# Kernel optimization log

Measured on AMD Instinct MI355X. Metric: run time of the kernel, lower is better.

The kernel has to match this reference:

```python
import jax, jax.numpy as jnp
import numpy as np

B, S, V, H, K, T = 4, 256, 32000, 1024, 4, 20
THRESHOLD = 0.6


def setup_inputs() -> dict:
    key = jax.random.key(0)
    ks = jax.random.split(key, 12)
    sH = 1.0 / np.sqrt(H)
    return {
        "input_ids": jax.random.randint(ks[0], (B, S), 0, V),
        "labels": jax.random.randint(ks[1], (B, S), 0, V),
        "embed": jax.random.normal(ks[2], (V, H), jnp.float32) * 0.02,
        "W1": jax.random.normal(ks[3], (H, H), jnp.float32) * sH,
        "b1": jnp.zeros((H,), jnp.float32),
        "lm_head": jax.random.normal(ks[4], (H, V), jnp.float32) * 0.02,
        "W_gen": jax.random.normal(ks[5], (H, H), jnp.float32) * sH,
        "thought_emb": jax.random.normal(ks[6], (K, H), jnp.float32) * 0.02,
        "tpos_emb": jax.random.normal(ks[7], (T, H), jnp.float32) * 0.02,
        "w_score": jax.random.normal(ks[8], (2 * H,), jnp.float32) * sH,
        "w_gate": jax.random.normal(ks[9], (2 * H,), jnp.float32) * sH,
    }


def reference(input_ids, labels, embed, W1, b1, lm_head, W_gen,
              thought_emb, tpos_emb, w_score, w_gate):
    # ---- base model: embed -> tanh MLP -> lm_head ----
    h0 = embed[input_ids]                                 # (B,S,H)
    hidden = jnp.tanh(h0 @ W1 + b1)                       # base last_hidden_state
    base_logits = hidden @ lm_head                        # (B,S,V)

    # ---- ThoughtInjector: per-position gate from normalized entropy ----
    logp = jax.nn.log_softmax(base_logits, axis=-1)
    ent = -jnp.sum(jnp.exp(logp) * logp, axis=-1) / jnp.log(float(V))  # (B,S)
    inject = (ent.mean(axis=0) > THRESHOLD) & (jnp.arange(S) < S - 1)   # (S,)

    # ---- ThoughtGenerator: (B,S,K,T,H) thoughts (masked dispatch, all pos) ----
    g = jnp.tanh(hidden @ W_gen)                          # (B,S,H)
    thoughts = jnp.tanh(g[:, :, None, None, :]
                        + thought_emb[None, None, :, None, :]
                        + tpos_emb[None, None, None, :, :])  # (B,S,K,T,H)
    tmean = thoughts.mean(axis=3)                         # (B,S,K,H) = thoughts.mean(dim=2)

    # ---- CoherenceScorer: composite score per thought ----
    comp = jax.nn.sigmoid(
        jnp.einsum('bsh,h->bs', hidden, w_score[:H])[:, :, None]
        + jnp.einsum('bskh,h->bsk', tmean, w_score[H:]))  # (B,S,K)

    # ---- MixingHead: coherence-weighted thought mix, gated blend with hidden ----
    alpha = jax.nn.softmax(comp, axis=-1)                 # (B,S,K)
    mixed_thought = jnp.einsum('bsk,bskh->bsh', alpha, tmean)
    gate = jax.nn.sigmoid(jnp.einsum('bsh,h->bs', hidden, w_gate[:H])
                          + jnp.einsum('bsh,h->bs', mixed_thought, w_gate[H:]))[..., None]
    mixed = gate * mixed_thought + (1.0 - gate) * hidden

    enhanced = jnp.where(inject[None, :, None], mixed, hidden)
    final_logits = enhanced @ lm_head                     # (B,S,V)

    # ---- shifted cross-entropy loss ----
    sl = jax.nn.log_softmax(final_logits[:, :-1, :], axis=-1)
    loss = -jnp.take_along_axis(sl, labels[:, 1:, None], axis=-1).mean()
    return final_logits, loss
```

## Files before the change

### kernel.cpp

```cpp
#include <hip/hip_runtime.h>


#define V_SZ 32000
#define H_SZ 1024
#define S_SZ 256
#define B_SZ 4
#define M_SZ 1024
#define K_TH 4
#define T_TH 20
#define NTILE_V 125
#define PARTS (NTILE_V * 4)

typedef __bf16 bf16_t;
typedef __bf16 bf16x8 __attribute__((ext_vector_type(8)));
typedef __bf16 bf16x4 __attribute__((ext_vector_type(4)));
typedef float  f32x4  __attribute__((ext_vector_type(4)));

typedef __attribute__((address_space(1))) void gvoid_t;
typedef __attribute__((address_space(3))) void lvoid_t;

__device__ __forceinline__ void async_copy16(const bf16_t* g, bf16_t* l) {
  __builtin_amdgcn_global_load_lds((gvoid_t*)g, (lvoid_t*)l, 16, 0, 0);
}

__device__ __forceinline__ float tanh_fast(float x) {
  x = fminf(fmaxf(x, -15.f), 15.f);
  float e = __expf(2.f * x);
  return (e - 1.f) / (e + 1.f);
}
__device__ __forceinline__ float sigmoid_f(float x) {
  return 1.f / (1.f + __expf(-x));
}

__device__ __forceinline__ void transpose_tile(
    const float* __restrict__ in, bf16_t* __restrict__ out, int R, int C,
    int bx, int by, float (*tile)[65], int t) {
  const int c0 = bx << 6, r0 = by << 6;
  const int tr = t >> 4, tc = (t & 15) << 2;
  #pragma unroll
  for (int i = 0; i < 4; ++i) {
    const float4 v = *(const float4*)(in + (size_t)(r0 + tr + 16 * i) * C + c0 + tc);
    tile[tr + 16 * i][tc]     = v.x;
    tile[tr + 16 * i][tc + 1] = v.y;
    tile[tr + 16 * i][tc + 2] = v.z;
    tile[tr + 16 * i][tc + 3] = v.w;
  }
  __syncthreads();
  const int wr = t >> 3, wc = (t & 7) << 3;
  #pragma unroll
  for (int i = 0; i < 2; ++i) {
    bf16x8 o;
    #pragma unroll
    for (int j = 0; j < 8; ++j) o[j] = (bf16_t)tile[wc + j][wr + 32 * i];
    *(bf16x8*)(out + (size_t)(c0 + wr + 32 * i) * R + r0 + wc) = o;
  }
}

__global__ void __launch_bounds__(256) prep_kernel(
    const float* __restrict__ lm, const float* __restrict__ W1,
    const float* __restrict__ Wg, const int* __restrict__ ids,
    const float* __restrict__ embed, bf16_t* __restrict__ lmT,
    bf16_t* __restrict__ W1T, bf16_t* __restrict__ WgT,
    bf16_t* __restrict__ X0) {
  __shared__ float tile[64][65];
  const int t = threadIdx.x;
  int bid = blockIdx.x;
  if (bid < 8000) {
    transpose_tile(lm, lmT, H_SZ, V_SZ, bid % 500, bid / 500, tile, t);
    return;
  }
  bid -= 8000;
  if (bid < 256) {
    transpose_tile(W1, W1T, H_SZ, H_SZ, bid % 16, bid / 16, tile, t);
    return;
  }
  bid -= 256;
  if (bid < 256) {
    transpose_tile(Wg, WgT, H_SZ, H_SZ, bid % 16, bid / 16, tile, t);
    return;
  }
  bid -= 256;
  const int i = bid * 256 + t;
  const int m = i >> 8, c4 = (i & 255) << 2;
  const float4 v = *(const float4*)(embed + (size_t)ids[m] * H_SZ + c4);
  bf16x4 o;
  o[0] = (bf16_t)v.x; o[1] = (bf16_t)v.y; o[2] = (bf16_t)v.z; o[3] = (bf16_t)v.w;
  *(bf16x4*)(X0 + (size_t)m * H_SZ + c4) = o;
}

template <int EPI>
__global__ void __launch_bounds__(256, 2) gemm_bt(
    const bf16_t* __restrict__ A, const bf16_t* __restrict__ BT,
    float* __restrict__ outF, bf16_t* __restrict__ outB,
    const float* __restrict__ bias, int mtiles, int ntiles, int N) {
  __shared__ __align__(16) bf16_t As[128 * 32];
  __shared__ __align__(16) bf16_t Bs[128 * 32];
  const int t = threadIdx.x;
  const int x = blockIdx.x & 7, y = blockIdx.x >> 3;
  const int tm = y % mtiles, tn = x + 8 * (y / mtiles);
  if (tn >= ntiles) return;
  const int m0 = tm * 128, n0 = tn * 128;
  const int lane = t & 63, wv = t >> 6, wm = wv >> 1, wn = wv & 1;
  const int col = lane & 15, qd = lane >> 4;

  const int srow = 16 * wv + (lane >> 2);
  const int schunk = ((lane & 3) ^ ((srow >> 1) & 3)) << 3;
  const bf16_t* gA0 = A  + (size_t)(m0 + srow) * 1024 + schunk;
  const bf16_t* gA1 = A  + (size_t)(m0 + srow + 64) * 1024 + schunk;
  const bf16_t* gB0 = BT + (size_t)(n0 + srow) * 1024 + schunk;
  const bf16_t* gB1 = BT + (size_t)(n0 + srow + 64) * 1024 + schunk;
  bf16_t* lA0 = As + wv * 512;
  bf16_t* lA1 = As + 2048 + wv * 512;
  bf16_t* lB0 = Bs + wv * 512;
  bf16_t* lB1 = Bs + 2048 + wv * 512;

  int offA[4], offB[4];
  #pragma unroll
  for (int i = 0; i < 4; ++i) {
    const int ra = wm * 64 + i * 16 + col;
    offA[i] = ra * 32 + ((qd ^ ((ra >> 1) & 3)) << 3);
    const int rb = wn * 64 + i * 16 + col;
    offB[i] = rb * 32 + ((qd ^ ((rb >> 1) & 3)) << 3);
  }
  f32x4 acc[4][4] = {};
  for (int kb = 0; kb < 1024; kb += 32) {
    async_copy16(gA0 + kb, lA0);
    async_copy16(gA1 + kb, lA1);
    async_copy16(gB0 + kb, lB0);
    async_copy16(gB1 + kb, lB1);
    __syncthreads();
    bf16x8 af[4], bg[4];
    #pragma unroll
    for (int mi = 0; mi < 4; ++mi) af[mi] = *(const bf16x8*)(As + offA[mi]);
    #pragma unroll
    for (int ni = 0; ni < 4; ++ni) bg[ni] = *(const bf16x8*)(Bs + offB[ni]);
    #pragma unroll
    for (int mi = 0; mi < 4; ++mi)
      #pragma unroll
      for (int ni = 0; ni < 4; ++ni)
        acc[mi][ni] = __builtin_amdgcn_mfma_f32_16x16x32_bf16(
            af[mi], bg[ni], acc[mi][ni], 0, 0, 0);
    __syncthreads();
  }
  #pragma unroll
  for (int mi = 0; mi < 4; ++mi) {
    #pragma unroll
    for (int ni = 0; ni < 4; ++ni) {
      const int gm = m0 + wm * 64 + mi * 16 + qd * 4;
      const int gn = n0 + wn * 64 + ni * 16 + col;
      #pragma unroll
      for (int r = 0; r < 4; ++r) {
        const size_t o = (size_t)(gm + r) * N + gn;
        float v = acc[mi][ni][r];
        if (EPI == 1) {
          v = tanh_fast(v + bias[gn]);
          outF[o] = v;
          outB[o] = (bf16_t)v;
        } else {
          outF[o] = tanh_fast(v);
        }
      }
    }
  }
}

template <int EPI>
__global__ void __launch_bounds__(512, 2) gemm_big(
    const bf16_t* __restrict__ A, const bf16_t* __restrict__ BT,
    float* __restrict__ outF, float2* __restrict__ entP,
    float* __restrict__ lseP, int mtiles, int ntiles, int N) {
  __shared__ __align__(16) bf16_t As[3][256 * 32];
  __shared__ __align__(16) bf16_t Bs[3][256 * 32];
  const int t = threadIdx.x;
  const int x = blockIdx.x & 7, y = blockIdx.x >> 3;
  const int tm = y % mtiles, tn = x + 8 * (y / mtiles);
  if (tn >= ntiles) return;
  const int m0 = tm * 256, n0 = tn * 256;
  const int lane = t & 63, wv = t >> 6;
  const int wm = wv >> 2, wn = wv & 3;
  const int col = lane & 15, qd = lane >> 4;

  int ldsOff[2], srow[2], sch[2];
  #pragma unroll
  for (int j = 0; j < 2; ++j) {
    const int cid = j * 512 + wv * 64 + lane;
    srow[j] = cid >> 2;
    sch[j] = ((cid & 3) ^ ((srow[j] >> 1) & 3)) << 3;
    ldsOff[j] = (j * 512 + wv * 64) * 8;
  }
  const bf16_t* gA0 = A  + (size_t)(m0 + srow[0]) * 1024 + sch[0];
  const bf16_t* gA1 = A  + (size_t)(m0 + srow[1]) * 1024 + sch[1];
  const bf16_t* gB0 = BT + (size_t)(n0 + srow[0]) * 1024 + sch[0];
  const bf16_t* gB1 = BT + (size_t)(n0 + srow[1]) * 1024 + sch[1];

  int offA[8], offB[4];
  #pragma unroll
  for (int i = 0; i < 8; ++i) {
    const int ra = wm * 128 + i * 16 + col;
    offA[i] = ra * 32 + ((qd ^ ((ra >> 1) & 3)) << 3);
  }
  #pragma unroll
  for (int i = 0; i < 4; ++i) {
    const int rb = wn * 64 + i * 16 + col;
    offB[i] = rb * 32 + ((qd ^ ((rb >> 1) & 3)) << 3);
  }

  f32x4 acc[8][4] = {};

  async_copy16(gA0, &As[0][ldsOff[0]]);
  async_copy16(gA1, &As[0][ldsOff[1]]);
  async_copy16(gB0, &Bs[0][ldsOff[0]]);
  async_copy16(gB1, &Bs[0][ldsOff[1]]);
  async_copy16(gA0 + 32, &As[1][ldsOff[0]]);
  async_copy16(gA1 + 32, &As[1][ldsOff[1]]);
  async_copy16(gB0 + 32, &Bs[1][ldsOff[0]]);
  async_copy16(gB1 + 32, &Bs[1][ldsOff[1]]);
  asm volatile("s_waitcnt vmcnt(4)" ::: "memory");
  __builtin_amdgcn_sched_barrier(0);
  __builtin_amdgcn_s_barrier();

  int cur = 0;
  for (int kt = 0; kt < 32; ++kt) {
    const bf16_t* __restrict__ Ab = &As[cur][0];
    const bf16_t* __restrict__ Bb = &Bs[cur][0];
    const int nb = (cur == 0) ? 2 : cur - 1;
    const int kb2 = (kt + 2) * 32;
    bf16x8 af[8], b0, b1;
    #pragma unroll
    for (int i = 0; i < 8; ++i) af[i] = *(const bf16x8*)(Ab + offA[i]);
    b0 = *(const bf16x8*)(Bb + offB[0]);
    b1 = *(const bf16x8*)(Bb + offB[1]);
    if (kt < 30) {
      async_copy16(gA0 + kb2, &As[nb][ldsOff[0]]);
      async_copy16(gA1 + kb2, &As[nb][ldsOff[1]]);
    }
    __builtin_amdgcn_s_barrier();
    __builtin_amdgcn_s_setprio(1);
    #pragma unroll
    for (int i = 0; i < 8; ++i) {
      acc[i][0] = __builtin_amdgcn_mfma_f32_16x16x32_bf16(af[i], b0, acc[i][0], 0, 0, 0);
      acc[i][1] = __builtin_amdgcn_mfma_f32_16x16x32_bf16(af[i], b1, acc[i][1], 0, 0, 0);
    }
    __builtin_amdgcn_s_setprio(0);
    __builtin_amdgcn_s_barrier();
    b0 = *(const bf16x8*)(Bb + offB[2]);
    b1 = *(const bf16x8*)(Bb + offB[3]);
    if (kt < 30) {
      async_copy16(gB0 + kb2, &Bs[nb][ldsOff[0]]);
      async_copy16(gB1 + kb2, &Bs[nb][ldsOff[1]]);
      asm volatile("s_waitcnt vmcnt(4)" ::: "memory");
    } else if (kt == 30) {
      asm volatile("s_waitcnt vmcnt(0)" ::: "memory");
    }
    __builtin_amdgcn_sched_barrier(0);
    __builtin_amdgcn_s_barrier();
    __builtin_amdgcn_s_setprio(1);
    #pragma unroll
    for (int i = 0; i < 8; ++i) {
      acc[i][2] = __builtin_amdgcn_mfma_f32_16x16x32_bf16(af[i], b0, acc[i][2], 0, 0, 0);
      acc[i][3] = __builtin_amdgcn_mfma_f32_16x16x32_bf16(af[i], b1, acc[i][3], 0, 0, 0);
    }
    __builtin_amdgcn_s_setprio(0);
    __builtin_amdgcn_s_barrier();
    cur = (cur == 2) ? 0 : cur + 1;
  }

  #pragma unroll
  for (int mi = 0; mi < 8; ++mi) {
    #pragma unroll
    for (int rr = 0; rr < 4; ++rr) {
      const int row = m0 + wm * 128 + mi * 16 + qd * 4 + rr;
      float zz = 0.f, ss = 0.f;
      #pragma unroll
      for (int ni = 0; ni < 4; ++ni) {
        const float xv = acc[mi][ni][rr];
        const float e = __expf(xv);
        zz += e;
        if (EPI == 3) ss += xv * e;
        if (EPI == 4)
          outF[(size_t)row * N + n0 + wn * 64 + ni * 16 + col] = xv;
      }
      #pragma unroll
      for (int d = 1; d < 16; d <<= 1) {
        zz += __shfl_xor(zz, d);
        if (EPI == 3) ss += __shfl_xor(ss, d);
      }
      if (col == 0) {
        if (EPI == 3)
          entP[(size_t)row * PARTS + tn * 4 + wn] = make_float2(zz, ss);
        else
          lseP[(size_t)row * PARTS + tn * 4 + wn] = zz;
      }
    }
  }
}

__global__ void __launch_bounds__(256) lse_merge_kernel(
    const float* __restrict__ lseP, float* __restrict__ lse) {
  const int t = threadIdx.x, w = t >> 6, lane = t & 63;
  const int row = blockIdx.x * 4 + w;
  float z = 0.f;
  for (int i = lane; i < PARTS; i += 64) z += lseP[(size_t)row * PARTS + i];
  #pragma unroll
  for (int d = 1; d < 64; d <<= 1) z += __shfl_xor(z, d);
  if (lane == 0) lse[row] = __logf(z);
}

__device__ __forceinline__ float block_sum(float v, float* red, int t) {
  red[t] = v;
  __syncthreads();
  for (int off = 128; off > 0; off >>= 1) {
    if (t < off) red[t] += red[t + off];
    __syncthreads();
  }
  const float r = red[0];
  __syncthreads();
  return r;
}

__global__ void __launch_bounds__(256) mix_kernel(
    const float* __restrict__ hidden, const float* __restrict__ gF,
    const float* __restrict__ th_emb, const float* __restrict__ tpos,
    const float* __restrict__ w_score, const float* __restrict__ w_gate,
    const float2* __restrict__ entP, bf16_t* __restrict__ enhB) {
  const int m = blockIdx.x, t = threadIdx.x, s = m & (S_SZ - 1);
  __shared__ float red[256];
  __shared__ float se[4];

  {
    const int w = t >> 6, lane = t & 63;
    const int row = w * S_SZ + s;
    float z = 0.f, sv = 0.f;
    for (int i = lane; i < PARTS; i += 64) {
      const float2 pz = entP[(size_t)row * PARTS + i];
      z += pz.x; sv += pz.y;
    }
    #pragma unroll
    for (int d = 1; d < 64; d <<= 1) {
      z += __shfl_xor(z, d);
      sv += __shfl_xor(sv, d);
    }
    if (lane == 0) se[w] = __logf(z) - sv / z;
    __syncthreads();
  }
  const float emean = 0.25f * (se[0] + se[1] + se[2] + se[3]);
  const int inj = (emean * (1.0f / 10.373491f) > 0.6f) && (s < S_SZ - 1);

  float hv[4], ws1[4], ws2[4], wg1[4], wg2[4], tmv[4][4];
  #pragma unroll
  for (int j = 0; j < 4; ++j) {
    const int h = t + 256 * j;
    hv[j]  = hidden[(size_t)m * H_SZ + h];
    ws1[j] = w_score[h];      ws2[j] = w_score[H_SZ + h];
    wg1[j] = w_gate[h];       wg2[j] = w_gate[H_SZ + h];
    const float gv = gF[(size_t)m * H_SZ + h];
    float tp[T_TH];
    #pragma unroll
    for (int tt = 0; tt < T_TH; ++tt) tp[tt] = tpos[tt * H_SZ + h];
    #pragma unroll
    for (int k = 0; k < 4; ++k) {
      const float base = gv + th_emb[k * H_SZ + h];
      float ssum = 0.f;
      #pragma unroll
      for (int tt = 0; tt < T_TH; ++tt) ssum += tanh_fast(base + tp[tt]);
      tmv[k][j] = ssum * (1.f / T_TH);
    }
  }
  float ph = 0.f, pg = 0.f;
  #pragma unroll
  for (int j = 0; j < 4; ++j) { ph += hv[j] * ws1[j]; pg += hv[j] * wg1[j]; }
  const float sh = block_sum(ph, red, t);
  const float gh = block_sum(pg, red, t);
  float comp[4];
  #pragma unroll
  for (int k = 0; k < 4; ++k) {
    float pc = 0.f;
    #pragma unroll
    for (int j = 0; j < 4; ++j) pc += tmv[k][j] * ws2[j];
    const float ck = block_sum(pc, red, t);
    comp[k] = sigmoid_f(sh + ck);
  }
  const float ma = fmaxf(fmaxf(comp[0], comp[1]), fmaxf(comp[2], comp[3]));
  float al[4], asum = 0.f;
  #pragma unroll
  for (int k = 0; k < 4; ++k) { al[k] = __expf(comp[k] - ma); asum += al[k]; }
  const float inv = 1.f / asum;
  float mx[4];
  #pragma unroll
  for (int j = 0; j < 4; ++j) {
    mx[j] = 0.f;
    #pragma unroll
    for (int k = 0; k < 4; ++k) mx[j] += al[k] * inv * tmv[k][j];
  }
  float pm = 0.f;
  #pragma unroll
  for (int j = 0; j < 4; ++j) pm += mx[j] * wg2[j];
  const float gm = block_sum(pm, red, t);
  const float gate = sigmoid_f(gh + gm);
  #pragma unroll
  for (int j = 0; j < 4; ++j) {
    const float e = inj ? (gate * mx[j] + (1.f - gate) * hv[j]) : hv[j];
    enhB[(size_t)m * H_SZ + t + 256 * j] = (bf16_t)e;
  }
}

__global__ void __launch_bounds__(256) loss_kernel(
    const float* __restrict__ logits, const float* __restrict__ lse,
    const int* __restrict__ labels, float* __restrict__ out_loss) {
  const int t = threadIdx.x;
  float acc = 0.f;
  for (int i = t; i < (S_SZ - 1) * B_SZ; i += 256) {
    const int b = i / (S_SZ - 1), s2 = i % (S_SZ - 1);
    const int m = b * S_SZ + s2;
    const int lab = labels[m + 1];
    acc += lse[m] - logits[(size_t)m * V_SZ + lab];
  }
  __shared__ float red[256];
  red[t] = acc;
  __syncthreads();
  for (int off = 128; off > 0; off >>= 1) {
    if (t < off) red[t] += red[t + off];
    __syncthreads();
  }
  if (t == 0) out_loss[0] = red[0] / (float)((S_SZ - 1) * B_SZ);
}

extern "C" void kernel_launch(void* const* d_in, const int* in_sizes, int n_in,
                              void* d_out, int out_size, void* d_ws, size_t ws_size,
                              hipStream_t stream) {
  const int*   ids    = (const int*)  d_in[0];
  const int*   labels = (const int*)  d_in[1];
  const float* embed  = (const float*)d_in[2];
  const float* W1     = (const float*)d_in[3];
  const float* b1     = (const float*)d_in[4];
  const float* lm     = (const float*)d_in[5];
  const float* Wg     = (const float*)d_in[6];
  const float* thE    = (const float*)d_in[7];
  const float* tpos   = (const float*)d_in[8];
  const float* wsc    = (const float*)d_in[9];
  const float* wgt    = (const float*)d_in[10];
  float* out = (float*)d_out;

  char* p = (char*)d_ws;
  auto carve = [&p](size_t bytes) {
    char* r = p;
    p += (bytes + 255) & ~(size_t)255;
    return r;
  };
  bf16_t* lmT   = (bf16_t*)carve((size_t)V_SZ * H_SZ * sizeof(bf16_t));
  bf16_t* W1T   = (bf16_t*)carve((size_t)H_SZ * H_SZ * sizeof(bf16_t));
  bf16_t* WgT   = (bf16_t*)carve((size_t)H_SZ * H_SZ * sizeof(bf16_t));
  bf16_t* X0    = (bf16_t*)carve((size_t)M_SZ * H_SZ * sizeof(bf16_t));
  bf16_t* hidB  = (bf16_t*)carve((size_t)M_SZ * H_SZ * sizeof(bf16_t));
  bf16_t* enhB  = (bf16_t*)carve((size_t)M_SZ * H_SZ * sizeof(bf16_t));
  float*  hidF  = (float*) carve((size_t)M_SZ * H_SZ * sizeof(float));
  float*  gF    = (float*) carve((size_t)M_SZ * H_SZ * sizeof(float));
  float*  partials = (float*)carve((size_t)M_SZ * PARTS * sizeof(float2));
  float*  lse   = (float*) carve(M_SZ * sizeof(float));
  float2* entP = (float2*)partials;
  float*  lseP = (float*)partials;

  prep_kernel<<<9536, 256, 0, stream>>>(lm, W1, Wg, ids, embed, lmT, W1T, WgT, X0);

  gemm_bt<1><<<64, 256, 0, stream>>>(X0, W1T, hidF, hidB, b1, 8, 8, H_SZ);
  gemm_bt<2><<<64, 256, 0, stream>>>(hidB, WgT, gF, nullptr, nullptr, 8, 8, H_SZ);
  gemm_big<3><<<512, 512, 0, stream>>>(hidB, lmT, nullptr, entP, nullptr, 4, NTILE_V, V_SZ);

  mix_kernel<<<M_SZ, 256, 0, stream>>>(hidF, gF, thE, tpos, wsc, wgt, entP, enhB);

  gemm_big<4><<<512, 512, 0, stream>>>(enhB, lmT, out, nullptr, lseP, 4, NTILE_V, V_SZ);
  lse_merge_kernel<<<M_SZ / 4, 256, 0, stream>>>(lseP, lse);
  loss_kernel<<<1, 256, 0, stream>>>(out, lse, labels, out + (size_t)M_SZ * V_SZ);
}
```

Before: 588.2 us.

## Retile small GEMMs, widen lm_head transpose tile, simplify big GEMM pipeline, fuse loss

The lm_head transpose now handles 128x64 tiles per block, cutting the block count in half. The H×H GEMMs switch from 128x128 tiles on 64 blocks to 64x64 double-buffered tiles on 256 blocks to fill more CUs. The big GEMM main loop drops the split half-B-fragment scheduling with mid-iteration barriers and loads all four B fragments before one MFMA burst. The lse merge and loss kernels become a single kernel that accumulates the loss with atomics, and the big GEMM zeroes the loss slot. This saves launches and improves occupancy, but it may lose MFMA/load interleaving in the big GEMM and makes the loss reduction order nondeterministic.

```diff
diff --git a/kernel.cpp b/kernel.cpp
--- a/kernel.cpp
+++ b/kernel.cpp
@@ -34,16 +34,16 @@
 
 __device__ __forceinline__ void transpose_tile(
     const float* __restrict__ in, bf16_t* __restrict__ out, int R, int C,
-    int bx, int by, float (*tile)[65], int t) {
+    int bx, int by, float* lds, int t) {
   const int c0 = bx << 6, r0 = by << 6;
   const int tr = t >> 4, tc = (t & 15) << 2;
   #pragma unroll
   for (int i = 0; i < 4; ++i) {
     const float4 v = *(const float4*)(in + (size_t)(r0 + tr + 16 * i) * C + c0 + tc);
-    tile[tr + 16 * i][tc]     = v.x;
-    tile[tr + 16 * i][tc + 1] = v.y;
-    tile[tr + 16 * i][tc + 2] = v.z;
-    tile[tr + 16 * i][tc + 3] = v.w;
+    lds[(tr + 16 * i) * 65 + tc]     = v.x;
+    lds[(tr + 16 * i) * 65 + tc + 1] = v.y;
+    lds[(tr + 16 * i) * 65 + tc + 2] = v.z;
+    lds[(tr + 16 * i) * 65 + tc + 3] = v.w;
   }
   __syncthreads();
   const int wr = t >> 3, wc = (t & 7) << 3;
@@ -51,7 +51,7 @@
   for (int i = 0; i < 2; ++i) {
     bf16x8 o;
     #pragma unroll
-    for (int j = 0; j < 8; ++j) o[j] = (bf16_t)tile[wc + j][wr + 32 * i];
+    for (int j = 0; j < 8; ++j) o[j] = (bf16_t)lds[(wc + j) * 65 + wr + 32 * i];
     *(bf16x8*)(out + (size_t)(c0 + wr + 32 * i) * R + r0 + wc) = o;
   }
 }
@@ -62,21 +62,42 @@
     const float* __restrict__ embed, bf16_t* __restrict__ lmT,
     bf16_t* __restrict__ W1T, bf16_t* __restrict__ WgT,
     bf16_t* __restrict__ X0) {
-  __shared__ float tile[64][65];
+  __shared__ float lds[64 * 129];
   const int t = threadIdx.x;
   int bid = blockIdx.x;
-  if (bid < 8000) {
-    transpose_tile(lm, lmT, H_SZ, V_SZ, bid % 500, bid / 500, tile, t);
+  if (bid < 4000) {
+    const int by = bid / 500, bx = bid % 500;
+    const int hr0 = by << 7, vc0 = bx << 6;
+    #pragma unroll
+    for (int j = 0; j < 8; ++j) {
+      const int idx = j * 256 + t;
+      const int r = idx >> 4, c4 = (idx & 15) << 2;
+      const float4 v = *(const float4*)(lm + (size_t)(hr0 + r) * V_SZ + vc0 + c4);
+      lds[(c4 + 0) * 129 + r] = v.x;
+      lds[(c4 + 1) * 129 + r] = v.y;
+      lds[(c4 + 2) * 129 + r] = v.z;
+      lds[(c4 + 3) * 129 + r] = v.w;
+    }
+    __syncthreads();
+    #pragma unroll
+    for (int j = 0; j < 4; ++j) {
+      const int idx = j * 256 + t;
+      const int i = idx >> 4, seg = idx & 15;
+      bf16x8 o;
+      #pragma unroll
+      for (int k = 0; k < 8; ++k) o[k] = (bf16_t)lds[i * 129 + seg * 8 + k];
+      *(bf16x8*)(lmT + (size_t)(vc0 + i) * H_SZ + hr0 + seg * 8) = o;
+    }
     return;
   }
-  bid -= 8000;
+  bid -= 4000;
   if (bid < 256) {
-    transpose_tile(W1, W1T, H_SZ, H_SZ, bid % 16, bid / 16, tile, t);
+    transpose_tile(W1, W1T, H_SZ, H_SZ, bid % 16, bid / 16, lds, t);
     return;
   }
   bid -= 256;
   if (bid < 256) {
-    transpose_tile(Wg, WgT, H_SZ, H_SZ, bid % 16, bid / 16, tile, t);
+    transpose_tile(Wg, WgT, H_SZ, H_SZ, bid % 16, bid / 16, lds, t);
     return;
   }
   bid -= 256;
@@ -89,68 +110,63 @@
 }
 
 template <int EPI>
-__global__ void __launch_bounds__(256, 2) gemm_bt(
+__global__ void __launch_bounds__(256) gemm_sm(
     const bf16_t* __restrict__ A, const bf16_t* __restrict__ BT,
     float* __restrict__ outF, bf16_t* __restrict__ outB,
-    const float* __restrict__ bias, int mtiles, int ntiles, int N) {
-  __shared__ __align__(16) bf16_t As[128 * 32];
-  __shared__ __align__(16) bf16_t Bs[128 * 32];
+    const float* __restrict__ bias) {
+  __shared__ __align__(16) bf16_t As[2][64 * 32];
+  __shared__ __align__(16) bf16_t Bs[2][64 * 32];
   const int t = threadIdx.x;
   const int x = blockIdx.x & 7, y = blockIdx.x >> 3;
-  const int tm = y % mtiles, tn = x + 8 * (y / mtiles);
-  if (tn >= ntiles) return;
-  const int m0 = tm * 128, n0 = tn * 128;
+  const int tm = y & 15, tn = x + 8 * (y >> 4);
+  const int m0 = tm * 64, n0 = tn * 64;
   const int lane = t & 63, wv = t >> 6, wm = wv >> 1, wn = wv & 1;
   const int col = lane & 15, qd = lane >> 4;
-
-  const int srow = 16 * wv + (lane >> 2);
-  const int schunk = ((lane & 3) ^ ((srow >> 1) & 3)) << 3;
-  const bf16_t* gA0 = A  + (size_t)(m0 + srow) * 1024 + schunk;
-  const bf16_t* gA1 = A  + (size_t)(m0 + srow + 64) * 1024 + schunk;
-  const bf16_t* gB0 = BT + (size_t)(n0 + srow) * 1024 + schunk;
-  const bf16_t* gB1 = BT + (size_t)(n0 + srow + 64) * 1024 + schunk;
-  bf16_t* lA0 = As + wv * 512;
-  bf16_t* lA1 = As + 2048 + wv * 512;
-  bf16_t* lB0 = Bs + wv * 512;
-  bf16_t* lB1 = Bs + 2048 + wv * 512;
-
-  int offA[4], offB[4];
-  #pragma unroll
-  for (int i = 0; i < 4; ++i) {
-    const int ra = wm * 64 + i * 16 + col;
+  const int srow = t >> 2;
+  const int sch = ((t & 3) ^ ((srow >> 1) & 3)) << 3;
+  const bf16_t* gA = A  + (size_t)(m0 + srow) * 1024 + sch;
+  const bf16_t* gB = BT + (size_t)(n0 + srow) * 1024 + sch;
+  const int ldso = wv * 512;
+  int offA[2], offB[2];
+  #pragma unroll
+  for (int i = 0; i < 2; ++i) {
+    const int ra = wm * 32 + i * 16 + col;
     offA[i] = ra * 32 + ((qd ^ ((ra >> 1) & 3)) << 3);
-    const int rb = wn * 64 + i * 16 + col;
+    const int rb = wn * 32 + i * 16 + col;
     offB[i] = rb * 32 + ((qd ^ ((rb >> 1) & 3)) << 3);
   }
-  f32x4 acc[4][4] = {};
-  for (int kb = 0; kb < 1024; kb += 32) {
-    async_copy16(gA0 + kb, lA0);
-    async_copy16(gA1 + kb, lA1);
-    async_copy16(gB0 + kb, lB0);
-    async_copy16(gB1 + kb, lB1);
-    __syncthreads();
-    bf16x8 af[4], bg[4];
-    #pragma unroll
-    for (int mi = 0; mi < 4; ++mi) af[mi] = *(const bf16x8*)(As + offA[mi]);
-    #pragma unroll
-    for (int ni = 0; ni < 4; ++ni) bg[ni] = *(const bf16x8*)(Bs + offB[ni]);
-    #pragma unroll
-    for (int mi = 0; mi < 4; ++mi)
-      #pragma unroll
-      for (int ni = 0; ni < 4; ++ni)
+  f32x4 acc[2][2] = {};
+  async_copy16(gA, &As[0][ldso]);
+  async_copy16(gB, &Bs[0][ldso]);
+  __syncthreads();
+  for (int kt = 0; kt < 32; ++kt) {
+    const int cur = kt & 1;
+    if (kt < 31) {
+      async_copy16(gA + (kt + 1) * 32, &As[cur ^ 1][ldso]);
+      async_copy16(gB + (kt + 1) * 32, &Bs[cur ^ 1][ldso]);
+    }
+    bf16x8 af[2], bg[2];
+    #pragma unroll
+    for (int i = 0; i < 2; ++i) af[i] = *(const bf16x8*)(&As[cur][0] + offA[i]);
+    #pragma unroll
+    for (int i = 0; i < 2; ++i) bg[i] = *(const bf16x8*)(&Bs[cur][0] + offB[i]);
+    #pragma unroll
+    for (int mi = 0; mi < 2; ++mi)
+      #pragma unroll
+      for (int ni = 0; ni < 2; ++ni)
         acc[mi][ni] = __builtin_amdgcn_mfma_f32_16x16x32_bf16(
             af[mi], bg[ni], acc[mi][ni], 0, 0, 0);
     __syncthreads();
   }
   #pragma unroll
-  for (int mi = 0; mi < 4; ++mi) {
-    #pragma unroll
-    for (int ni = 0; ni < 4; ++ni) {
-      const int gm = m0 + wm * 64 + mi * 16 + qd * 4;
-      const int gn = n0 + wn * 64 + ni * 16 + col;
+  for (int mi = 0; mi < 2; ++mi) {
+    #pragma unroll
+    for (int ni = 0; ni < 2; ++ni) {
+      const int gm = m0 + wm * 32 + mi * 16 + qd * 4;
+      const int gn = n0 + wn * 32 + ni * 16 + col;
       #pragma unroll
       for (int r = 0; r < 4; ++r) {
-        const size_t o = (size_t)(gm + r) * N + gn;
+        const size_t o = (size_t)(gm + r) * 1024 + gn;
         float v = acc[mi][ni][r];
         if (EPI == 1) {
           v = tanh_fast(v + bias[gn]);
@@ -168,30 +184,33 @@
 __global__ void __launch_bounds__(512, 2) gemm_big(
     const bf16_t* __restrict__ A, const bf16_t* __restrict__ BT,
     float* __restrict__ outF, float2* __restrict__ entP,
-    float* __restrict__ lseP, int mtiles, int ntiles, int N) {
+    float* __restrict__ lseP, float* __restrict__ lossZ) {
   __shared__ __align__(16) bf16_t As[3][256 * 32];
   __shared__ __align__(16) bf16_t Bs[3][256 * 32];
   const int t = threadIdx.x;
   const int x = blockIdx.x & 7, y = blockIdx.x >> 3;
-  const int tm = y % mtiles, tn = x + 8 * (y / mtiles);
-  if (tn >= ntiles) return;
+  const int tm = y & 3, tn = x + 8 * (y >> 2);
+  if (EPI == 4 && blockIdx.x == 0 && t == 0) lossZ[0] = 0.f;
+  if (tn >= NTILE_V) return;
   const int m0 = tm * 256, n0 = tn * 256;
   const int lane = t & 63, wv = t >> 6;
   const int wm = wv >> 2, wn = wv & 3;
   const int col = lane & 15, qd = lane >> 4;
 
-  int ldsOff[2], srow[2], sch[2];
-  #pragma unroll
-  for (int j = 0; j < 2; ++j) {
-    const int cid = j * 512 + wv * 64 + lane;
-    srow[j] = cid >> 2;
-    sch[j] = ((cid & 3) ^ ((srow[j] >> 1) & 3)) << 3;
-    ldsOff[j] = (j * 512 + wv * 64) * 8;
-  }
-  const bf16_t* gA0 = A  + (size_t)(m0 + srow[0]) * 1024 + sch[0];
-  const bf16_t* gA1 = A  + (size_t)(m0 + srow[1]) * 1024 + sch[1];
-  const bf16_t* gB0 = BT + (size_t)(n0 + srow[0]) * 1024 + sch[0];
-  const bf16_t* gB1 = BT + (size_t)(n0 + srow[1]) * 1024 + sch[1];
+  int ldsOff0, ldsOff1, sch0, sch1, sr0, sr1;
+  {
+    const int cid0 = wv * 64 + lane;
+    const int cid1 = 512 + wv * 64 + lane;
+    sr0 = cid0 >> 2; sr1 = cid1 >> 2;
+    sch0 = ((cid0 & 3) ^ ((sr0 >> 1) & 3)) << 3;
+    sch1 = ((cid1 & 3) ^ ((sr1 >> 1) & 3)) << 3;
+    ldsOff0 = (wv * 64) * 8;
+    ldsOff1 = (512 + wv * 64) * 8;
+  }
+  const bf16_t* gA0 = A  + (size_t)(m0 + sr0) * 1024 + sch0;
+  const bf16_t* gA1 = A  + (size_t)(m0 + sr1) * 1024 + sch1;
+  const bf16_t* gB0 = BT + (size_t)(n0 + sr0) * 1024 + sch0;
+  const bf16_t* gB1 = BT + (size_t)(n0 + sr1) * 1024 + sch1;
 
   int offA[8], offB[4];
   #pragma unroll
@@ -207,61 +226,50 @@
 
   f32x4 acc[8][4] = {};
 
-  async_copy16(gA0, &As[0][ldsOff[0]]);
-  async_copy16(gA1, &As[0][ldsOff[1]]);
-  async_copy16(gB0, &Bs[0][ldsOff[0]]);
-  async_copy16(gB1, &Bs[0][ldsOff[1]]);
-  async_copy16(gA0 + 32, &As[1][ldsOff[0]]);
-  async_copy16(gA1 + 32, &As[1][ldsOff[1]]);
-  async_copy16(gB0 + 32, &Bs[1][ldsOff[0]]);
-  async_copy16(gB1 + 32, &Bs[1][ldsOff[1]]);
+  #pragma unroll
+  for (int pt = 0; pt < 2; ++pt) {
+    async_copy16(gA0 + pt * 32, &As[pt][ldsOff0]);
+    async_copy16(gA1 + pt * 32, &As[pt][ldsOff1]);
+    async_copy16(gB0 + pt * 32, &Bs[pt][ldsOff0]);
+    async_copy16(gB1 + pt * 32, &Bs[pt][ldsOff1]);
+  }
   asm volatile("s_waitcnt vmcnt(4)" ::: "memory");
   __builtin_amdgcn_sched_barrier(0);
   __builtin_amdgcn_s_barrier();
+  asm volatile("" ::: "memory");
 
   int cur = 0;
   for (int kt = 0; kt < 32; ++kt) {
-    const bf16_t* __restrict__ Ab = &As[cur][0];
-    const bf16_t* __restrict__ Bb = &Bs[cur][0];
-    const int nb = (cur == 0) ? 2 : cur - 1;
-    const int kb2 = (kt + 2) * 32;
-    bf16x8 af[8], b0, b1;
+    const bf16_t* Ab = &As[cur][0];
+    const bf16_t* Bb = &Bs[cur][0];
+    bf16x8 af[8], bg[4];
     #pragma unroll
     for (int i = 0; i < 8; ++i) af[i] = *(const bf16x8*)(Ab + offA[i]);
-    b0 = *(const bf16x8*)(Bb + offB[0]);
-    b1 = *(const bf16x8*)(Bb + offB[1]);
+    #pragma unroll
+    for (int i = 0; i < 4; ++i) bg[i] = *(const bf16x8*)(Bb + offB[i]);
     if (kt < 30) {
-      async_copy16(gA0 + kb2, &As[nb][ldsOff[0]]);
-      async_copy16(gA1 + kb2, &As[nb][ldsOff[1]]);
-    }
-    __builtin_amdgcn_s_barrier();
-    __builtin_amdgcn_s_setprio(1);
-    #pragma unroll
-    for (int i = 0; i < 8; ++i) {
-      acc[i][0] = __builtin_amdgcn_mfma_f32_16x16x32_bf16(af[i], b0, acc[i][0], 0, 0, 0);
-      acc[i][1] = __builtin_amdgcn_mfma_f32_16x16x32_bf16(af[i], b1, acc[i][1], 0, 0, 0);
-    }
-    __builtin_amdgcn_s_setprio(0);
-    __builtin_amdgcn_s_barrier();
-    b0 = *(const bf16x8*)(Bb + offB[2]);
-    b1 = *(const bf16x8*)(Bb + offB[3]);
-    if (kt < 30) {
-      async_copy16(gB0 + kb2, &Bs[nb][ldsOff[0]]);
-      async_copy16(gB1 + kb2, &Bs[nb][ldsOff[1]]);
+      const int nb = (cur == 0) ? 2 : cur - 1;
+      const int kb2 = (kt + 2) * 32;
+      async_copy16(gA0 + kb2, &As[nb][ldsOff0]);
+      async_copy16(gA1 + kb2, &As[nb][ldsOff1]);
+      async_copy16(gB0 + kb2, &Bs[nb][ldsOff0]);
+      async_copy16(gB1 + kb2, &Bs[nb][ldsOff1]);
       asm volatile("s_waitcnt vmcnt(4)" ::: "memory");
-    } else if (kt == 30) {
+    } else {
       asm volatile("s_waitcnt vmcnt(0)" ::: "memory");
     }
     __builtin_amdgcn_sched_barrier(0);
     __builtin_amdgcn_s_barrier();
     __builtin_amdgcn_s_setprio(1);
     #pragma unroll
-    for (int i = 0; i < 8; ++i) {
-      acc[i][2] = __builtin_amdgcn_mfma_f32_16x16x32_bf16(af[i], b0, acc[i][2], 0, 0, 0);
-      acc[i][3] = __builtin_amdgcn_mfma_f32_16x16x32_bf16(af[i], b1, acc[i][3], 0, 0, 0);
-    }
+    for (int mi = 0; mi < 8; ++mi)
+      #pragma unroll
+      for (int ni = 0; ni < 4; ++ni)
+        acc[mi][ni] = __builtin_amdgcn_mfma_f32_16x16x32_bf16(
+            af[mi], bg[ni], acc[mi][ni], 0, 0, 0);
     __builtin_amdgcn_s_setprio(0);
     __builtin_amdgcn_s_barrier();
+    asm volatile("" ::: "memory");
     cur = (cur == 2) ? 0 : cur + 1;
   }
 
@@ -278,7 +286,7 @@
         zz += e;
         if (EPI == 3) ss += xv * e;
         if (EPI == 4)
-          outF[(size_t)row * N + n0 + wn * 64 + ni * 16 + col] = xv;
+          outF[(size_t)row * V_SZ + n0 + wn * 64 + ni * 16 + col] = xv;
       }
       #pragma unroll
       for (int d = 1; d < 16; d <<= 1) {
@@ -295,15 +303,24 @@
   }
 }
 
-__global__ void __launch_bounds__(256) lse_merge_kernel(
-    const float* __restrict__ lseP, float* __restrict__ lse) {
+__global__ void __launch_bounds__(256) lse_loss_kernel(
+    const float* __restrict__ lseP, const float* __restrict__ logits,
+    const int* __restrict__ labels, float* __restrict__ out_loss) {
   const int t = threadIdx.x, w = t >> 6, lane = t & 63;
   const int row = blockIdx.x * 4 + w;
   float z = 0.f;
   for (int i = lane; i < PARTS; i += 64) z += lseP[(size_t)row * PARTS + i];
   #pragma unroll
   for (int d = 1; d < 64; d <<= 1) z += __shfl_xor(z, d);
-  if (lane == 0) lse[row] = __logf(z);
+  if (lane == 0) {
+    const int s = row & (S_SZ - 1);
+    if (s < S_SZ - 1) {
+      const float lse = __logf(z);
+      const int lab = labels[row + 1];
+      const float term = lse - logits[(size_t)row * V_SZ + lab];
+      atomicAdd(out_loss, term * (1.f / (float)((S_SZ - 1) * B_SZ)));
+    }
+  }
 }
 
 __device__ __forceinline__ float block_sum(float v, float* red, int t) {
@@ -402,27 +419,6 @@
     const float e = inj ? (gate * mx[j] + (1.f - gate) * hv[j]) : hv[j];
     enhB[(size_t)m * H_SZ + t + 256 * j] = (bf16_t)e;
   }
-}
-
-__global__ void __launch_bounds__(256) loss_kernel(
-    const float* __restrict__ logits, const float* __restrict__ lse,
-    const int* __restrict__ labels, float* __restrict__ out_loss) {
-  const int t = threadIdx.x;
-  float acc = 0.f;
-  for (int i = t; i < (S_SZ - 1) * B_SZ; i += 256) {
-    const int b = i / (S_SZ - 1), s2 = i % (S_SZ - 1);
-    const int m = b * S_SZ + s2;
-    const int lab = labels[m + 1];
-    acc += lse[m] - logits[(size_t)m * V_SZ + lab];
-  }
-  __shared__ float red[256];
-  red[t] = acc;
-  __syncthreads();
-  for (int off = 128; off > 0; off >>= 1) {
-    if (t < off) red[t] += red[t + off];
-    __syncthreads();
-  }
-  if (t == 0) out_loss[0] = red[0] / (float)((S_SZ - 1) * B_SZ);
 }
 
 extern "C" void kernel_launch(void* const* d_in, const int* in_sizes, int n_in,
@@ -456,19 +452,18 @@
   float*  hidF  = (float*) carve((size_t)M_SZ * H_SZ * sizeof(float));
   float*  gF    = (float*) carve((size_t)M_SZ * H_SZ * sizeof(float));
   float*  partials = (float*)carve((size_t)M_SZ * PARTS * sizeof(float2));
-  float*  lse   = (float*) carve(M_SZ * sizeof(float));
   float2* entP = (float2*)partials;
   float*  lseP = (float*)partials;
-
-  prep_kernel<<<9536, 256, 0, stream>>>(lm, W1, Wg, ids, embed, lmT, W1T, WgT, X0);
-
-  gemm_bt<1><<<64, 256, 0, stream>>>(X0, W1T, hidF, hidB, b1, 8, 8, H_SZ);
-  gemm_bt<2><<<64, 256, 0, stream>>>(hidB, WgT, gF, nullptr, nullptr, 8, 8, H_SZ);
-  gemm_big<3><<<512, 512, 0, stream>>>(hidB, lmT, nullptr, entP, nullptr, 4, NTILE_V, V_SZ);
+  float*  lossOut = out + (size_t)M_SZ * V_SZ;
+
+  prep_kernel<<<5536, 256, 0, stream>>>(lm, W1, Wg, ids, embed, lmT, W1T, WgT, X0);
+
+  gemm_sm<1><<<256, 256, 0, stream>>>(X0, W1T, hidF, hidB, b1);
+  gemm_sm<2><<<256, 256, 0, stream>>>(hidB, WgT, gF, nullptr, nullptr);
+  gemm_big<3><<<512, 512, 0, stream>>>(hidB, lmT, nullptr, entP, nullptr, nullptr);
 
   mix_kernel<<<M_SZ, 256, 0, stream>>>(hidF, gF, thE, tpos, wsc, wgt, entP, enhB);
 
-  gemm_big<4><<<512, 512, 0, stream>>>(enhB, lmT, out, nullptr, lseP, 4, NTILE_V, V_SZ);
-  lse_merge_kernel<<<M_SZ / 4, 256, 0, stream>>>(lseP, lse);
-  loss_kernel<<<1, 256, 0, stream>>>(out, lse, labels, out + (size_t)M_SZ * V_SZ);
-}
+  gemm_big<4><<<512, 512, 0, stream>>>(enhB, lmT, out, nullptr, lseP, lossOut);
+  lse_loss_kernel<<<M_SZ / 4, 256, 0, stream>>>(lseP, out, labels, lossOut);
+}
```

New measurement: 694.9 us. 18.1% more time.
